# Optimization experiments

Measured on AMD Instinct MI355X. Metric: run time of the kernel, lower is better.

Reference implementation:

```python
import jax, jax.numpy as jnp
import numpy as np

IN_DIM = 1024
LOW_D_FF = 128
OUT_DIM = 1024
B = 8
S = 2048

def _xavier_normal(key, shape):
    fan_in, fan_out = shape[1], shape[0]
    std = float(np.sqrt(2.0 / (fan_in + fan_out)))
    return jax.random.normal(key, shape, dtype=jnp.float32) * std

def setup_inputs() -> dict:
    key = jax.random.key(0)
    kx, kk, kd, ku = jax.random.split(key, 4)
    x = jax.random.normal(kx, (B, S, IN_DIM), dtype=jnp.float32)
    k = jax.random.normal(kk, (B, LOW_D_FF), dtype=jnp.float32)
    D_matrix = _xavier_normal(kd, (IN_DIM * LOW_D_FF, LOW_D_FF))
    U_matrix = _xavier_normal(ku, (LOW_D_FF * OUT_DIM, LOW_D_FF))
    return {"x": x, "k": k, "D_matrix": D_matrix, "U_matrix": U_matrix}

def reference(x, k, D_matrix, U_matrix):
    # x: [B, S, in_dim], k: [B, low_d_ff]
    Bn = x.shape[0]
    low = k.shape[-1]
    # hypernetwork weight generation: per-sample D [B, in_dim, low], U [B, low, out_dim]
    D = jnp.einsum('pk,bk->bp', D_matrix, k).reshape(Bn, IN_DIM, low)
    U = jnp.einsum('pk,bk->bp', U_matrix, k).reshape(Bn, low, OUT_DIM)
    h = jax.nn.relu(jnp.einsum('bsd,bdl->bsl', x, D))
    return jnp.einsum('bsl,blo->bso', h, U)
```

## Files before the change

kernel.cpp:

```cpp
#include <hip/hip_runtime.h>
#include <hip/hip_bf16.h>
#include <stdint.h>

#define IN_DIM  1024
#define LOW     128
#define OUT_DIM 1024
#define BATCH   8
#define SEQ     2048

typedef unsigned short u16;
typedef short bf16x8 __attribute__((ext_vector_type(8)));
typedef unsigned short u16x4 __attribute__((ext_vector_type(4)));
typedef float f32x4 __attribute__((ext_vector_type(4)));

__device__ __forceinline__ u16 f2bf(float f) {
    union { float f; uint32_t u; } v;
    v.f = f;
    uint32_t u = v.u;
    return (u16)((u + 0x7fffu + ((u >> 16) & 1u)) >> 16);
}

__device__ __forceinline__ void gload16(const float* g, float* l) {
    __builtin_amdgcn_global_load_lds(
        (const __attribute__((address_space(1))) void*)g,
        (__attribute__((address_space(3))) void*)l, 16, 0, 0);
}

__global__ __launch_bounds__(256) void gen_w(const float* __restrict__ Dm,
                                             const float* __restrict__ Um,
                                             const float* __restrict__ kv,
                                             u16* __restrict__ DgT,
                                             u16* __restrict__ UgT) {
    __shared__ float sbuf[2][64 * 128];
    __shared__ u16 tb[8 * 8 * 32];

    int t = threadIdx.x;
    int bid = blockIdx.x;
    bool isU = bid >= 512;
    int rb = isU ? (bid - 512) : bid;
    const float* src = isU ? Um : Dm;
    u16* outp = isU ? UgT : DgT;
    int NTOT = isU ? 1024 : 128;
    int MTOT = isU ? 128 : 1024;
    int sh = isU ? 7 : 4;
    int m0 = (rb >> sh) * 32;
    int n0 = (rb & ((1 << sh) - 1)) * 8;

    int g8 = t >> 5;
    int srcChunk = (t & 31) ^ g8;
    const float* gbase = src + ((size_t)m0 * NTOT + n0 + g8) * 128 + srcChunk * 4;
    size_t mstep = (size_t)NTOT * 128;

    int lane = t & 63, w = t >> 6;
    int bb = lane & 15;
    int hi = lane >> 4;
    int rsw = lane & 7;

    bf16x8 bfrag[4];
#pragma unroll
    for (int ks = 0; ks < 4; ++ks)
#pragma unroll
        for (int j = 0; j < 8; ++j) {
            float kvf = (bb < 8) ? kv[bb * LOW + ks * 32 + hi * 8 + j] : 0.f;
            bfrag[ks][j] = (short)f2bf(kvf);
        }

    {
        float* l0 = &sbuf[0][t * 4];
#pragma unroll
        for (int i = 0; i < 8; ++i)
            gload16(gbase + (size_t)i * mstep, l0 + i * 1024);
    }

    for (int c = 0; c < 4; ++c) {
        __syncthreads();
        if (c < 3) {
            float* ln = &sbuf[(c + 1) & 1][t * 4];
            const float* gn = gbase + (size_t)(8 * (c + 1)) * mstep;
#pragma unroll
            for (int i = 0; i < 8; ++i)
                gload16(gn + (size_t)i * mstep, ln + i * 1024);
        }
        const float* rowp = sbuf[c & 1] + (w * 16 + bb) * 128;
        f32x4 acc = (f32x4){0.f, 0.f, 0.f, 0.f};
#pragma unroll
        for (int ks = 0; ks < 4; ++ks) {
            int c0 = ks * 8 + hi * 2;
            f32x4 v0 = *(const f32x4*)(rowp + ((c0)     ^ rsw) * 4);
            f32x4 v1 = *(const f32x4*)(rowp + ((c0 + 1) ^ rsw) * 4);
            bf16x8 afr;
            afr[0] = (short)f2bf(v0.x); afr[1] = (short)f2bf(v0.y);
            afr[2] = (short)f2bf(v0.z); afr[3] = (short)f2bf(v0.w);
            afr[4] = (short)f2bf(v1.x); afr[5] = (short)f2bf(v1.y);
            afr[6] = (short)f2bf(v1.z); afr[7] = (short)f2bf(v1.w);
            acc = __builtin_amdgcn_mfma_f32_16x16x32_bf16(afr, bfrag[ks], acc, 0, 0, 0);
        }
        if (bb < 8) {
#pragma unroll
            for (int j = 0; j < 4; ++j) {
                int r = hi * 4 + j;
                int mm = c * 8 + w * 2 + (r >> 3);
                tb[bb * 256 + (r & 7) * 32 + mm] = f2bf(acc[j]);
            }
        }
    }
    __syncthreads();

    int c64 = t >> 2, q4 = t & 3;
    int bw = c64 >> 3, np = c64 & 7;
    bf16x8 v = *(const bf16x8*)(tb + bw * 256 + np * 32 + q4 * 8);
    *(bf16x8*)(outp + ((size_t)(bw * NTOT + n0 + np)) * MTOT + m0 + q4 * 8) = v;
}

__global__ __launch_bounds__(256) void fc1(const float* __restrict__ x,
                                           const u16* __restrict__ DgT,
                                           u16* __restrict__ h) {
    __shared__ u16 As[32][72];
    __shared__ u16 Bs[128][72];
    int t = threadIdx.x;
    int bid = blockIdx.x;
    int b = bid >> 6, st = bid & 63;
    int s0 = st * 32;
    const float* xb = x + ((size_t)b * SEQ + s0) * IN_DIM;
    const u16* Db = DgT + (size_t)b * LOW * IN_DIM;

    int w = t >> 6, lane = t & 63;
    int wm = w >> 1, wn = w & 1;
    int lr = lane & 15, hi = lane >> 4;

    f32x4 acc[4];
#pragma unroll
    for (int nf = 0; nf < 4; ++nf) acc[nf] = (f32x4){0.f, 0.f, 0.f, 0.f};

    int ar = t >> 3, ac = t & 7;
    int brt = t >> 3, bc = t & 7;

    for (int kt = 0; kt < IN_DIM / 64; ++kt) {
        int k0 = kt * 64;
#pragma unroll
        for (int i = 0; i < 2; ++i) {
            float4 v = *(const float4*)(xb + (size_t)ar * IN_DIM + k0 + ac * 4 + i * 32);
            u16x4 o;
            o.x = f2bf(v.x); o.y = f2bf(v.y); o.z = f2bf(v.z); o.w = f2bf(v.w);
            *(u16x4*)(&As[ar][ac * 4 + i * 32]) = o;
        }
#pragma unroll
        for (int i = 0; i < 4; ++i) {
            int row = brt + 32 * i;
            bf16x8 v = *(const bf16x8*)(Db + (size_t)row * IN_DIM + k0 + bc * 8);
            *(bf16x8*)(&Bs[row][bc * 8]) = v;
        }
        __syncthreads();
#pragma unroll
        for (int ks = 0; ks < 2; ++ks) {
            int kk = ks * 32 + hi * 8;
            bf16x8 af = *(const bf16x8*)(&As[wm * 16 + lr][kk]);
#pragma unroll
            for (int nf = 0; nf < 4; ++nf) {
                bf16x8 bf = *(const bf16x8*)(&Bs[wn * 64 + nf * 16 + lr][kk]);
                acc[nf] = __builtin_amdgcn_mfma_f32_16x16x32_bf16(af, bf, acc[nf], 0, 0, 0);
            }
        }
        __syncthreads();
    }
    u16* hb = h + ((size_t)b * SEQ + s0) * LOW;
#pragma unroll
    for (int nf = 0; nf < 4; ++nf) {
        int col = wn * 64 + nf * 16 + lr;
#pragma unroll
        for (int j = 0; j < 4; ++j) {
            int rrow = wm * 16 + hi * 4 + j;
            hb[(size_t)rrow * LOW + col] = f2bf(fmaxf(acc[nf][j], 0.f));
        }
    }
}

__global__ __launch_bounds__(256) void fc2(const u16* __restrict__ h,
                                           const u16* __restrict__ UgT,
                                           float* __restrict__ out) {
    __shared__ u16 As[128 * 128];
    __shared__ u16 Bs[128 * 128];
    int t = threadIdx.x;
    int bid = blockIdx.x;
    int b = bid >> 7, st = (bid >> 3) & 15, ot = bid & 7;
    int s0 = st * 128, o0 = ot * 128;
    const u16* hb = h + ((size_t)b * SEQ + s0) * LOW;
    const u16* Ub = UgT + ((size_t)b * OUT_DIM + o0) * LOW;

#pragma unroll
    for (int i = 0; i < 8; ++i) {
        int ch = i * 256 + t;
        int row = ch >> 4, c = ch & 15;
        int swc = c ^ (row & 7);
        *(bf16x8*)(As + row * 128 + swc * 8) = *(const bf16x8*)(hb + (size_t)ch * 8);
        *(bf16x8*)(Bs + row * 128 + swc * 8) = *(const bf16x8*)(Ub + (size_t)ch * 8);
    }
    __syncthreads();

    int w = t >> 6, lane = t & 63;
    int wm = w >> 1, wn = w & 1;
    int lr = lane & 15, lkc = (lane >> 4);

    f32x4 acc[4][4];
#pragma unroll
    for (int mf = 0; mf < 4; ++mf)
#pragma unroll
        for (int nf = 0; nf < 4; ++nf)
            acc[mf][nf] = (f32x4){0.f, 0.f, 0.f, 0.f};

#pragma unroll
    for (int ks = 0; ks < 4; ++ks) {
        bf16x8 af[4], bfr[4];
#pragma unroll
        for (int mf = 0; mf < 4; ++mf) {
            int row = wm * 64 + mf * 16 + lr;
            int swc = (ks * 4 + lkc) ^ (row & 7);
            af[mf] = *(const bf16x8*)(As + row * 128 + swc * 8);
        }
#pragma unroll
        for (int nf = 0; nf < 4; ++nf) {
            int row = wn * 64 + nf * 16 + lr;
            int swc = (ks * 4 + lkc) ^ (row & 7);
            bfr[nf] = *(const bf16x8*)(Bs + row * 128 + swc * 8);
        }
#pragma unroll
        for (int mf = 0; mf < 4; ++mf)
#pragma unroll
            for (int nf = 0; nf < 4; ++nf)
                acc[mf][nf] = __builtin_amdgcn_mfma_f32_16x16x32_bf16(
                    af[mf], bfr[nf], acc[mf][nf], 0, 0, 0);
    }

    float* ob = out + ((size_t)b * SEQ + s0) * OUT_DIM + o0;
#pragma unroll
    for (int mf = 0; mf < 4; ++mf)
#pragma unroll
        for (int nf = 0; nf < 4; ++nf) {
            int col = wn * 64 + nf * 16 + lr;
#pragma unroll
            for (int j = 0; j < 4; ++j) {
                int rrow = wm * 64 + mf * 16 + (lane >> 4) * 4 + j;
                ob[(size_t)rrow * OUT_DIM + col] = acc[mf][nf][j];
            }
        }
}

extern "C" void kernel_launch(void* const* d_in, const int* in_sizes, int n_in,
                              void* d_out, int out_size, void* d_ws, size_t ws_size,
                              hipStream_t stream) {
    const float* x  = (const float*)d_in[0];
    const float* kv = (const float*)d_in[1];
    const float* Dm = (const float*)d_in[2];
    const float* Um = (const float*)d_in[3];
    float* out = (float*)d_out;

    u16* DgT = (u16*)d_ws;
    u16* UgT = DgT + (size_t)BATCH * LOW * IN_DIM;
    u16* hbuf = UgT + (size_t)BATCH * OUT_DIM * LOW;

    gen_w<<<dim3(1024), dim3(256), 0, stream>>>(Dm, Um, kv, DgT, UgT);
    fc1<<<dim3(512), dim3(256), 0, stream>>>(x, DgT, hbuf);
    fc2<<<dim3(1024), dim3(256), 0, stream>>>(hbuf, UgT, out);
}
```

Before: 71.39 us.

## Load hypernetwork weight rows straight to registers with nontemporal loads, split generation kernel

The weight-generation kernel no longer stages D/U matrix rows through double-buffered LDS with global_load_lds. Each thread now issues all of its nontemporal vector loads up front into registers, then converts them and runs the MFMAs. The single fused launch is split into two launches, one for D and one for U, with occupancy hinted at one block per SM. This aims to remove the LDS round trip and barriers on a bandwidth-bound streaming read. In exchange it uses many more registers, adds a kernel launch, and may lose coalescing compared with the swizzled LDS staging.

```diff
diff --git a/kernel.cpp b/kernel.cpp
--- a/kernel.cpp
+++ b/kernel.cpp
@@ -20,90 +20,71 @@
     return (u16)((u + 0x7fffu + ((u >> 16) & 1u)) >> 16);
 }
 
-__device__ __forceinline__ void gload16(const float* g, float* l) {
-    __builtin_amdgcn_global_load_lds(
-        (const __attribute__((address_space(1))) void*)g,
-        (__attribute__((address_space(3))) void*)l, 16, 0, 0);
-}
-
-__global__ __launch_bounds__(256) void gen_w(const float* __restrict__ Dm,
-                                             const float* __restrict__ Um,
-                                             const float* __restrict__ kv,
-                                             u16* __restrict__ DgT,
-                                             u16* __restrict__ UgT) {
-    __shared__ float sbuf[2][64 * 128];
+__global__ __launch_bounds__(256, 1) void gen_half(const float* __restrict__ src,
+                                                   const float* __restrict__ kv,
+                                                   u16* __restrict__ outp,
+                                                   int NTOT, int MTOT, int sh) {
     __shared__ u16 tb[8 * 8 * 32];
 
     int t = threadIdx.x;
-    int bid = blockIdx.x;
-    bool isU = bid >= 512;
-    int rb = isU ? (bid - 512) : bid;
-    const float* src = isU ? Um : Dm;
-    u16* outp = isU ? UgT : DgT;
-    int NTOT = isU ? 1024 : 128;
-    int MTOT = isU ? 128 : 1024;
-    int sh = isU ? 7 : 4;
+    int rb = blockIdx.x;
     int m0 = (rb >> sh) * 32;
     int n0 = (rb & ((1 << sh) - 1)) * 8;
 
-    int g8 = t >> 5;
-    int srcChunk = (t & 31) ^ g8;
-    const float* gbase = src + ((size_t)m0 * NTOT + n0 + g8) * 128 + srcChunk * 4;
-    size_t mstep = (size_t)NTOT * 128;
-
     int lane = t & 63, w = t >> 6;
-    int bb = lane & 15;
+    int lr = lane & 15;
     int hi = lane >> 4;
-    int rsw = lane & 7;
 
     bf16x8 bfrag[4];
 #pragma unroll
     for (int ks = 0; ks < 4; ++ks)
 #pragma unroll
         for (int j = 0; j < 8; ++j) {
-            float kvf = (bb < 8) ? kv[bb * LOW + ks * 32 + hi * 8 + j] : 0.f;
+            float kvf = (lr < 8) ? kv[lr * LOW + ks * 32 + hi * 8 + j] : 0.f;
             bfrag[ks][j] = (short)f2bf(kvf);
         }
 
-    {
-        float* l0 = &sbuf[0][t * 4];
-#pragma unroll
-        for (int i = 0; i < 8; ++i)
-            gload16(gbase + (size_t)i * mstep, l0 + i * 1024);
-    }
-
-    for (int c = 0; c < 4; ++c) {
-        __syncthreads();
-        if (c < 3) {
-            float* ln = &sbuf[(c + 1) & 1][t * 4];
-            const float* gn = gbase + (size_t)(8 * (c + 1)) * mstep;
-#pragma unroll
-            for (int i = 0; i < 8; ++i)
-                gload16(gn + (size_t)i * mstep, ln + i * 1024);
-        }
-        const float* rowp = sbuf[c & 1] + (w * 16 + bb) * 128;
+    const float* abase = src +
+        ((size_t)(m0 + w * 8 + (lr >> 3)) * NTOT + n0 + (lr & 7)) * 128 + hi * 8;
+    size_t tstep = (size_t)2 * NTOT * 128;
+
+    f32x4 L[4][8];
+#pragma unroll
+    for (int tau = 0; tau < 4; ++tau) {
+        const float* rp = abase + (size_t)tau * tstep;
+#pragma unroll
+        for (int ks = 0; ks < 4; ++ks) {
+            L[tau][2 * ks] =
+                __builtin_nontemporal_load((const f32x4*)(rp + ks * 32));
+            L[tau][2 * ks + 1] =
+                __builtin_nontemporal_load((const f32x4*)(rp + ks * 32 + 4));
+        }
+    }
+
+#pragma unroll
+    for (int tau = 0; tau < 4; ++tau) {
         f32x4 acc = (f32x4){0.f, 0.f, 0.f, 0.f};
 #pragma unroll
         for (int ks = 0; ks < 4; ++ks) {
-            int c0 = ks * 8 + hi * 2;
-            f32x4 v0 = *(const f32x4*)(rowp + ((c0)     ^ rsw) * 4);
-            f32x4 v1 = *(const f32x4*)(rowp + ((c0 + 1) ^ rsw) * 4);
+            f32x4 v0 = L[tau][2 * ks], v1 = L[tau][2 * ks + 1];
             bf16x8 afr;
             afr[0] = (short)f2bf(v0.x); afr[1] = (short)f2bf(v0.y);
             afr[2] = (short)f2bf(v0.z); afr[3] = (short)f2bf(v0.w);
             afr[4] = (short)f2bf(v1.x); afr[5] = (short)f2bf(v1.y);
             afr[6] = (short)f2bf(v1.z); afr[7] = (short)f2bf(v1.w);
-            acc = __builtin_amdgcn_mfma_f32_16x16x32_bf16(afr, bfrag[ks], acc, 0, 0, 0);
-        }
-        if (bb < 8) {
+            acc = __builtin_amdgcn_mfma_f32_16x16x32_bf16(afr, bfrag[ks],
+                                                          acc, 0, 0, 0);
+        }
+        if (lr < 8) {
 #pragma unroll
             for (int j = 0; j < 4; ++j) {
                 int r = hi * 4 + j;
-                int mm = c * 8 + w * 2 + (r >> 3);
-                tb[bb * 256 + (r & 7) * 32 + mm] = f2bf(acc[j]);
+                int mm = w * 8 + tau * 2 + (r >> 3);
+                tb[lr * 256 + (r & 7) * 32 + mm] = f2bf(acc[j]);
             }
         }
     }
+
     __syncthreads();
 
     int c64 = t >> 2, q4 = t & 3;
@@ -254,11 +235,12 @@
     const float* Um = (const float*)d_in[3];
     float* out = (float*)d_out;
 
-    u16* DgT = (u16*)d_ws;
-    u16* UgT = DgT + (size_t)BATCH * LOW * IN_DIM;
+    u16* DgT  = (u16*)d_ws;
+    u16* UgT  = DgT + (size_t)BATCH * LOW * IN_DIM;
     u16* hbuf = UgT + (size_t)BATCH * OUT_DIM * LOW;
 
-    gen_w<<<dim3(1024), dim3(256), 0, stream>>>(Dm, Um, kv, DgT, UgT);
+    gen_half<<<dim3(512), dim3(256), 0, stream>>>(Dm, kv, DgT, 128, 1024, 4);
+    gen_half<<<dim3(512), dim3(256), 0, stream>>>(Um, kv, UgT, 1024, 128, 7);
     fc1<<<dim3(512), dim3(256), 0, stream>>>(x, DgT, hbuf);
     fc2<<<dim3(1024), dim3(256), 0, stream>>>(hbuf, UgT, out);
 }
```

Result: no change. 71.54 us (+0.2%).
